# Optimization experiments

Hardware: AMD Instinct MI355X
Metric: run time of the kernel (lower is better)

Reference implementation:

```python
import jax, jax.numpy as jnp
import numpy as np

B, S, H, NH, L, NS = 8, 4096, 768, 12, 2, 64
DH = H // NH
EPS = 1e-12


def _layer_norm(x, g, b):
    mu = jnp.mean(x, axis=-1, keepdims=True)
    var = jnp.mean((x - mu) ** 2, axis=-1, keepdims=True)
    return (x - mu) / jnp.sqrt(var + EPS) * g + b


def setup_inputs() -> dict:
    key = jax.random.key(0)
    ks = jax.random.split(key, 8)
    # sentence index per token: 64 equal contiguous sentences; position 0 is [CLS] in sentence 0
    sent_ind = jnp.broadcast_to((jnp.arange(S, dtype=jnp.int32) * NS) // S, (B, S)).astype(jnp.int32)
    start_layer = jax.random.normal(ks[0], (B, S, H), dtype=jnp.float32)
    init = lambda k, shape: (jax.random.normal(k, shape, dtype=jnp.float32) * 0.02)
    return {
        "sent_ind": sent_ind,
        "start_layer": start_layer,
        "Wq": init(ks[1], (L, H, H)), "bq": jnp.zeros((L, H), jnp.float32),
        "Wk": init(ks[2], (L, H, H)), "bk": jnp.zeros((L, H), jnp.float32),
        "Wv": init(ks[3], (L, H, H)), "bv": jnp.zeros((L, H), jnp.float32),
        "Wo": init(ks[4], (L, H, H)), "bo": jnp.zeros((L, H), jnp.float32),
        "ln_g": jnp.ones((L, H), jnp.float32), "ln_b": jnp.zeros((L, H), jnp.float32),
    }


def reference(sent_ind, start_layer, Wq, bq, Wk, bk, Wv, bv, Wo, bo, ln_g, ln_b):
    # ---- segment-mean pooling by sentence index (vectorized replacement of the python loops) ----
    onehot = (sent_ind[..., None] == jnp.arange(NS, dtype=sent_ind.dtype)).astype(start_layer.dtype)  # [B,S,NS]
    # the first [CLS] token is excluded from sentence 0's mean
    onehot = onehot.at[:, 0, :].set(0.0)
    sums = jnp.einsum('bsn,bsd->bnd', onehot, start_layer)          # [B,NS,H]
    counts = jnp.sum(onehot, axis=1)                                 # [B,NS]
    x = sums / counts[..., None]                                     # graph_vectors [B,NS,H]

    # ---- GAT layers: BertSelfAttention + GATSelfOutput(dense->gelu->LayerNorm), dropout=eval ----
    scale = 1.0 / (DH ** 0.5)
    for i in range(L):
        q = (x @ Wq[i] + bq[i]).reshape(B, NS, NH, DH)
        k = (x @ Wk[i] + bk[i]).reshape(B, NS, NH, DH)
        v = (x @ Wv[i] + bv[i]).reshape(B, NS, NH, DH)
        scores = jnp.einsum('bqhd,bkhd->bhqk', q, k) * scale
        probs = jax.nn.softmax(scores, axis=-1)
        ctx = jnp.einsum('bhqk,bkhd->bqhd', probs, v).reshape(B, NS, H)
        h = jax.nn.gelu(ctx @ Wo[i] + bo[i], approximate=False)
        x = _layer_norm(h, ln_g[i], ln_b[i])
    return x
```

## Files before the change

kernel.cpp:

```cpp
#include <hip/hip_runtime.h>
#include <hip/hip_bf16.h>

constexpr int cB  = 8;
constexpr int cS  = 4096;
constexpr int cH  = 768;
constexpr int cNH = 12;
constexpr int cL  = 2;
constexpr int cNS = 64;
constexpr int cDH = 64;
constexpr int cM  = cB * cNS;

typedef __attribute__((ext_vector_type(8))) short bf16x8;
typedef __attribute__((ext_vector_type(4))) float f32x4;

union PrepShared {
    float T[64][65];
    struct { int cnt; int list[cS]; } p;
};

__global__ __launch_bounds__(256) void prep_kernel(
    const int* __restrict__ sent_ind, const float* __restrict__ sl,
    __hip_bfloat16* __restrict__ xb,
    const float* __restrict__ Wq, const float* __restrict__ Wk,
    const float* __restrict__ Wv, const float* __restrict__ Wo,
    __hip_bfloat16* __restrict__ wt)
{
    __shared__ PrepShared sh;
    int tid = threadIdx.x;

    if (blockIdx.x < (unsigned)cM) {
        int bn = blockIdx.x;
        int b = bn >> 6, n = bn & (cNS - 1);
        if (tid == 0) sh.p.cnt = 0;
        __syncthreads();
        const int* si = sent_ind + (size_t)b * cS;
        for (int s = tid; s < cS; s += 256)
            if (s != 0 && si[s] == n) { int p = atomicAdd(&sh.p.cnt, 1); sh.p.list[p] = s; }
        __syncthreads();
        int c = sh.p.cnt;
        if (tid < 192) {
            const float* bbase = sl + (size_t)b * cS * cH;
            int col = tid * 4;
            float4 a0 = {0.f, 0.f, 0.f, 0.f};
            float4 a1 = {0.f, 0.f, 0.f, 0.f};
            float4 a2 = {0.f, 0.f, 0.f, 0.f};
            float4 a3 = {0.f, 0.f, 0.f, 0.f};
            int i = 0;
            for (; i + 4 <= c; i += 4) {
                float4 r0 = *(const float4*)(bbase + (size_t)sh.p.list[i + 0] * cH + col);
                float4 r1 = *(const float4*)(bbase + (size_t)sh.p.list[i + 1] * cH + col);
                float4 r2 = *(const float4*)(bbase + (size_t)sh.p.list[i + 2] * cH + col);
                float4 r3 = *(const float4*)(bbase + (size_t)sh.p.list[i + 3] * cH + col);
                a0.x += r0.x; a0.y += r0.y; a0.z += r0.z; a0.w += r0.w;
                a1.x += r1.x; a1.y += r1.y; a1.z += r1.z; a1.w += r1.w;
                a2.x += r2.x; a2.y += r2.y; a2.z += r2.z; a2.w += r2.w;
                a3.x += r3.x; a3.y += r3.y; a3.z += r3.z; a3.w += r3.w;
            }
            for (; i < c; ++i) {
                float4 r0 = *(const float4*)(bbase + (size_t)sh.p.list[i] * cH + col);
                a0.x += r0.x; a0.y += r0.y; a0.z += r0.z; a0.w += r0.w;
            }
            float inv = 1.0f / (float)c;
            __hip_bfloat16* xr = xb + (size_t)bn * cH + col;
            xr[0] = __float2bfloat16((a0.x + a1.x + a2.x + a3.x) * inv);
            xr[1] = __float2bfloat16((a0.y + a1.y + a2.y + a3.y) * inv);
            xr[2] = __float2bfloat16((a0.z + a1.z + a2.z + a3.z) * inv);
            xr[3] = __float2bfloat16((a0.w + a1.w + a2.w + a3.w) * inv);
        }
    } else {
        int bi = blockIdx.x - cM;
        int bx = bi % 12, by = (bi / 12) % 12, mat = bi / 144;
        int layer = mat >> 2, which = mat & 3;
        const float* W = (which == 0 ? Wq : which == 1 ? Wk : which == 2 ? Wv : Wo)
                         + (size_t)layer * cH * cH;
        int k0 = by * 64, n0 = bx * 64;
        int r = tid >> 2, cb = (tid & 3) * 16;
        #pragma unroll
        for (int u = 0; u < 4; ++u) {
            float4 w4 = *(const float4*)(W + (size_t)(k0 + r) * cH + n0 + cb + u * 4);
            sh.T[r][cb + u * 4 + 0] = w4.x; sh.T[r][cb + u * 4 + 1] = w4.y;
            sh.T[r][cb + u * 4 + 2] = w4.z; sh.T[r][cb + u * 4 + 3] = w4.w;
        }
        __syncthreads();
        int kk = tid & 63;
        int nb = (tid >> 6) * 16;
        __hip_bfloat16* dst = wt + ((size_t)mat * cH + n0) * cH + k0;
        #pragma unroll
        for (int u = 0; u < 16; ++u) {
            int nn = nb + u;
            dst[(size_t)nn * cH + kk] = __float2bfloat16(sh.T[kk][nn]);
        }
    }
}

template<int ACT>
__global__ __launch_bounds__(256) void gemm_mfma(
    const __hip_bfloat16* __restrict__ A,
    const __hip_bfloat16* __restrict__ Wt0,
    const float* __restrict__ biasA, const float* __restrict__ biasB,
    const float* __restrict__ biasC,
    float* __restrict__ C0)
{
    constexpr int K = cH, N = cH;
    int mat = blockIdx.z;
    const __hip_bfloat16* Wt = Wt0 + (size_t)mat * cH * cH;
    const float* bias = (mat == 0) ? biasA : (mat == 1) ? biasB : biasC;
    float* C = C0 + (size_t)mat * cM * cH;

    int lane = threadIdx.x & 63;
    int wave = threadIdx.x >> 6;
    int l15 = lane & 15, q = lane >> 4;
    int m0 = blockIdx.y * 64 + wave * 16;
    int n0 = blockIdx.x * 32;

    const __hip_bfloat16* Arow = A  + (size_t)(m0 + l15) * K + q * 8;
    const __hip_bfloat16* Wr0  = Wt + (size_t)(n0 + l15) * K + q * 8;
    const __hip_bfloat16* Wr1  = Wr0 + (size_t)16 * K;

    f32x4 acc0 = {0.f, 0.f, 0.f, 0.f};
    f32x4 acc1 = {0.f, 0.f, 0.f, 0.f};
    #pragma unroll 8
    for (int k0 = 0; k0 < K; k0 += 32) {
        bf16x8 a  = *(const bf16x8*)(Arow + k0);
        bf16x8 b0 = *(const bf16x8*)(Wr0 + k0);
        bf16x8 b1 = *(const bf16x8*)(Wr1 + k0);
        acc0 = __builtin_amdgcn_mfma_f32_16x16x32_bf16(a, b0, acc0, 0, 0, 0);
        acc1 = __builtin_amdgcn_mfma_f32_16x16x32_bf16(a, b1, acc1, 0, 0, 0);
    }
    #pragma unroll
    for (int nt = 0; nt < 2; ++nt) {
        const f32x4 acc = nt == 0 ? acc0 : acc1;
        int col = n0 + nt * 16 + l15;
        float bv = bias[col];
        #pragma unroll
        for (int r = 0; r < 4; ++r) {
            int row = m0 + q * 4 + r;
            float v = acc[r] + bv;
            if (ACT == 1) v = 0.5f * v * (1.0f + erff(v * 0.70710678118654752f));
            C[(size_t)row * N + col] = v;
        }
    }
}

__global__ __launch_bounds__(256) void attn_kernel(
    const float* __restrict__ q, const float* __restrict__ k,
    const float* __restrict__ v, __hip_bfloat16* __restrict__ ctx)
{
    int bh = blockIdx.x;
    int b = bh / cNH, hh = bh % cNH;
    __shared__ float Qs[cNS][cDH + 4];
    __shared__ float Ks[cNS][cDH + 4];
    __shared__ float Vt[cDH][cNS + 4];
    __shared__ float Ps[cNS][cNS + 4];
    int tid = threadIdx.x;
    size_t base = ((size_t)b * cNS) * cH + hh * cDH;

    for (int i = tid; i < cNS * cDH / 4; i += 256) {
        int r = i >> 4;
        int c = (i & 15) << 2;
        float4 qv = *(const float4*)(q + base + (size_t)r * cH + c);
        float4 kv = *(const float4*)(k + base + (size_t)r * cH + c);
        float4 vv = *(const float4*)(v + base + (size_t)r * cH + c);
        *(float4*)&Qs[r][c] = qv;
        *(float4*)&Ks[r][c] = kv;
        Vt[c + 0][r] = vv.x; Vt[c + 1][r] = vv.y;
        Vt[c + 2][r] = vv.z; Vt[c + 3][r] = vv.w;
    }
    __syncthreads();

    int tx = tid & 15, ty = tid >> 4;
    float accs[4][4] = {};
    for (int d = 0; d < cDH; d += 4) {
        float4 qv[4], kv[4];
        #pragma unroll
        for (int i = 0; i < 4; ++i) qv[i] = *(const float4*)&Qs[ty * 4 + i][d];
        #pragma unroll
        for (int j = 0; j < 4; ++j) kv[j] = *(const float4*)&Ks[tx + j * 16][d];
        #pragma unroll
        for (int i = 0; i < 4; ++i)
            #pragma unroll
            for (int j = 0; j < 4; ++j)
                accs[i][j] += qv[i].x * kv[j].x + qv[i].y * kv[j].y +
                              qv[i].z * kv[j].z + qv[i].w * kv[j].w;
    }
    const float scale = 0.125f;
    #pragma unroll
    for (int i = 0; i < 4; ++i)
        #pragma unroll
        for (int j = 0; j < 4; ++j)
            Ps[ty * 4 + i][tx + j * 16] = accs[i][j] * scale;
    __syncthreads();

    {
        int row = tid >> 2, jq = tid & 3;
        float e[16];
        float m = -1e30f;
        #pragma unroll
        for (int c = 0; c < 16; ++c) { e[c] = Ps[row][jq * 16 + c]; m = fmaxf(m, e[c]); }
        m = fmaxf(m, __shfl_xor(m, 1));
        m = fmaxf(m, __shfl_xor(m, 2));
        float s = 0.f;
        #pragma unroll
        for (int c = 0; c < 16; ++c) { e[c] = __expf(e[c] - m); s += e[c]; }
        s += __shfl_xor(s, 1);
        s += __shfl_xor(s, 2);
        float inv = 1.0f / s;
        #pragma unroll
        for (int c = 0; c < 16; ++c) Ps[row][jq * 16 + c] = e[c] * inv;
    }
    __syncthreads();

    float acco[4][4] = {};
    for (int c = 0; c < cNS; c += 4) {
        float4 p4[4], vt4[4];
        #pragma unroll
        for (int i = 0; i < 4; ++i) p4[i] = *(const float4*)&Ps[ty * 4 + i][c];
        #pragma unroll
        for (int j = 0; j < 4; ++j) vt4[j] = *(const float4*)&Vt[tx + j * 16][c];
        #pragma unroll
        for (int i = 0; i < 4; ++i)
            #pragma unroll
            for (int j = 0; j < 4; ++j)
                acco[i][j] += p4[i].x * vt4[j].x + p4[i].y * vt4[j].y +
                              p4[i].z * vt4[j].z + p4[i].w * vt4[j].w;
    }
    #pragma unroll
    for (int i = 0; i < 4; ++i)
        #pragma unroll
        for (int j = 0; j < 4; ++j)
            ctx[base + (size_t)(ty * 4 + i) * cH + tx + j * 16] =
                __float2bfloat16(acco[i][j]);
}

__global__ __launch_bounds__(256) void ln_kernel(
    const float* __restrict__ h, const float* __restrict__ g,
    const float* __restrict__ bb, __hip_bfloat16* __restrict__ xb,
    float* __restrict__ outf)
{
    int row = blockIdx.x;
    const float* r = h + (size_t)row * cH;
    int tid = threadIdx.x;
    float v0 = r[tid], v1 = r[tid + 256], v2 = r[tid + 512];
    float s = v0 + v1 + v2;
    __shared__ float red[4];
    #pragma unroll
    for (int o = 32; o; o >>= 1) s += __shfl_xor(s, o);
    if ((tid & 63) == 0) red[tid >> 6] = s;
    __syncthreads();
    float mu = (red[0] + red[1] + red[2] + red[3]) * (1.0f / 768.0f);
    float d0 = v0 - mu, d1 = v1 - mu, d2 = v2 - mu;
    float ss = d0 * d0 + d1 * d1 + d2 * d2;
    __syncthreads();
    #pragma unroll
    for (int o = 32; o; o >>= 1) ss += __shfl_xor(ss, o);
    if ((tid & 63) == 0) red[tid >> 6] = ss;
    __syncthreads();
    float var = (red[0] + red[1] + red[2] + red[3]) * (1.0f / 768.0f);
    float inv = rsqrtf(var + 1e-12f);
    float o0 = d0 * inv * g[tid]       + bb[tid];
    float o1 = d1 * inv * g[tid + 256] + bb[tid + 256];
    float o2 = d2 * inv * g[tid + 512] + bb[tid + 512];
    __hip_bfloat16* xr = xb + (size_t)row * cH;
    xr[tid]       = __float2bfloat16(o0);
    xr[tid + 256] = __float2bfloat16(o1);
    xr[tid + 512] = __float2bfloat16(o2);
    if (outf) {
        float* orow = outf + (size_t)row * cH;
        orow[tid] = o0; orow[tid + 256] = o1; orow[tid + 512] = o2;
    }
}

extern "C" void kernel_launch(void* const* d_in, const int* in_sizes, int n_in,
                              void* d_out, int out_size, void* d_ws, size_t ws_size,
                              hipStream_t stream) {
    const int*   sent_ind = (const int*)d_in[0];
    const float* start    = (const float*)d_in[1];
    const float* Wq = (const float*)d_in[2];
    const float* bq = (const float*)d_in[3];
    const float* Wk = (const float*)d_in[4];
    const float* bk = (const float*)d_in[5];
    const float* Wv = (const float*)d_in[6];
    const float* bv = (const float*)d_in[7];
    const float* Wo = (const float*)d_in[8];
    const float* bo = (const float*)d_in[9];
    const float* ln_g = (const float*)d_in[10];
    const float* ln_b = (const float*)d_in[11];
    float* out = (float*)d_out;

    char* w = (char*)d_ws;
    __hip_bfloat16* wt     = (__hip_bfloat16*)w;
    __hip_bfloat16* x_bf   = (__hip_bfloat16*)(w + 9437184);
    __hip_bfloat16* ctx_bf = (__hip_bfloat16*)(w + 9437184 + 786432);
    float* qb = (float*)(w + 9437184 + 2 * 786432);
    float* hb = qb + (size_t)3 * cM * cH;

    prep_kernel<<<cM + 1152, 256, 0, stream>>>(sent_ind, start, x_bf,
                                               Wq, Wk, Wv, Wo, wt);

    for (int i = 0; i < cL; ++i) {
        const __hip_bfloat16* wtq = wt + (size_t)(i * 4 + 0) * cH * cH;
        const __hip_bfloat16* wto = wt + (size_t)(i * 4 + 3) * cH * cH;
        gemm_mfma<0><<<dim3(24, 8, 3), 256, 0, stream>>>(
            x_bf, wtq, bq + (size_t)i * cH, bk + (size_t)i * cH, bv + (size_t)i * cH, qb);
        attn_kernel<<<cB * cNH, 256, 0, stream>>>(
            qb, qb + (size_t)cM * cH, qb + (size_t)2 * cM * cH, ctx_bf);
        gemm_mfma<1><<<dim3(24, 8, 1), 256, 0, stream>>>(
            ctx_bf, wto, bo + (size_t)i * cH, nullptr, nullptr, hb);
        ln_kernel<<<cM, 256, 0, stream>>>(hb, ln_g + (size_t)i * cH, ln_b + (size_t)i * cH,
                                          x_bf, (i == cL - 1) ? out : nullptr);
    }
}
```

Baseline: 292.5 us.

## Fuse all stages into one persistent cooperative kernel with grid syncs

Replaces the prep, QKV GEMM, attention, output GEMM and LayerNorm launches with a single cooperative kernel of 256 blocks. Each phase loops over its work items and phases are separated by grid.sync, with one shared-memory union reused across phases. The aim is to remove per-launch overhead and the gaps between the nine kernels. The cost is that the bandwidth-heavy pooling and weight-transpose phase now runs on only 256 resident blocks instead of over 1600, which may hurt latency hiding. Grid-wide barriers also add their own cost.

```diff
diff --git a/kernel.cpp b/kernel.cpp
--- a/kernel.cpp
+++ b/kernel.cpp
@@ -1,5 +1,8 @@
 #include <hip/hip_runtime.h>
 #include <hip/hip_bf16.h>
+#include <hip/hip_cooperative_groups.h>
+
+namespace cg = cooperative_groups;
 
 constexpr int cB  = 8;
 constexpr int cS  = 4096;
@@ -9,118 +12,34 @@
 constexpr int cNS = 64;
 constexpr int cDH = 64;
 constexpr int cM  = cB * cNS;
+constexpr int cG  = 256;
 
 typedef __attribute__((ext_vector_type(8))) short bf16x8;
 typedef __attribute__((ext_vector_type(4))) float f32x4;
 
-union PrepShared {
+union SharedU {
+    struct { int cnt; int list[cS]; } p;
     float T[64][65];
-    struct { int cnt; int list[cS]; } p;
+    struct { float QP[64][68]; float Ks[64][68]; float Vt[64][68]; } a;
 };
 
-__global__ __launch_bounds__(256) void prep_kernel(
-    const int* __restrict__ sent_ind, const float* __restrict__ sl,
-    __hip_bfloat16* __restrict__ xb,
-    const float* __restrict__ Wq, const float* __restrict__ Wk,
-    const float* __restrict__ Wv, const float* __restrict__ Wo,
-    __hip_bfloat16* __restrict__ wt)
+__device__ inline void gemm_tile(const __hip_bfloat16* __restrict__ A,
+                                 const __hip_bfloat16* __restrict__ Wt,
+                                 const float* __restrict__ bias,
+                                 float* __restrict__ C,
+                                 int bx, int by, int l15, int q4, int wave,
+                                 bool gelu)
 {
-    __shared__ PrepShared sh;
-    int tid = threadIdx.x;
-
-    if (blockIdx.x < (unsigned)cM) {
-        int bn = blockIdx.x;
-        int b = bn >> 6, n = bn & (cNS - 1);
-        if (tid == 0) sh.p.cnt = 0;
-        __syncthreads();
-        const int* si = sent_ind + (size_t)b * cS;
-        for (int s = tid; s < cS; s += 256)
-            if (s != 0 && si[s] == n) { int p = atomicAdd(&sh.p.cnt, 1); sh.p.list[p] = s; }
-        __syncthreads();
-        int c = sh.p.cnt;
-        if (tid < 192) {
-            const float* bbase = sl + (size_t)b * cS * cH;
-            int col = tid * 4;
-            float4 a0 = {0.f, 0.f, 0.f, 0.f};
-            float4 a1 = {0.f, 0.f, 0.f, 0.f};
-            float4 a2 = {0.f, 0.f, 0.f, 0.f};
-            float4 a3 = {0.f, 0.f, 0.f, 0.f};
-            int i = 0;
-            for (; i + 4 <= c; i += 4) {
-                float4 r0 = *(const float4*)(bbase + (size_t)sh.p.list[i + 0] * cH + col);
-                float4 r1 = *(const float4*)(bbase + (size_t)sh.p.list[i + 1] * cH + col);
-                float4 r2 = *(const float4*)(bbase + (size_t)sh.p.list[i + 2] * cH + col);
-                float4 r3 = *(const float4*)(bbase + (size_t)sh.p.list[i + 3] * cH + col);
-                a0.x += r0.x; a0.y += r0.y; a0.z += r0.z; a0.w += r0.w;
-                a1.x += r1.x; a1.y += r1.y; a1.z += r1.z; a1.w += r1.w;
-                a2.x += r2.x; a2.y += r2.y; a2.z += r2.z; a2.w += r2.w;
-                a3.x += r3.x; a3.y += r3.y; a3.z += r3.z; a3.w += r3.w;
-            }
-            for (; i < c; ++i) {
-                float4 r0 = *(const float4*)(bbase + (size_t)sh.p.list[i] * cH + col);
-                a0.x += r0.x; a0.y += r0.y; a0.z += r0.z; a0.w += r0.w;
-            }
-            float inv = 1.0f / (float)c;
-            __hip_bfloat16* xr = xb + (size_t)bn * cH + col;
-            xr[0] = __float2bfloat16((a0.x + a1.x + a2.x + a3.x) * inv);
-            xr[1] = __float2bfloat16((a0.y + a1.y + a2.y + a3.y) * inv);
-            xr[2] = __float2bfloat16((a0.z + a1.z + a2.z + a3.z) * inv);
-            xr[3] = __float2bfloat16((a0.w + a1.w + a2.w + a3.w) * inv);
-        }
-    } else {
-        int bi = blockIdx.x - cM;
-        int bx = bi % 12, by = (bi / 12) % 12, mat = bi / 144;
-        int layer = mat >> 2, which = mat & 3;
-        const float* W = (which == 0 ? Wq : which == 1 ? Wk : which == 2 ? Wv : Wo)
-                         + (size_t)layer * cH * cH;
-        int k0 = by * 64, n0 = bx * 64;
-        int r = tid >> 2, cb = (tid & 3) * 16;
-        #pragma unroll
-        for (int u = 0; u < 4; ++u) {
-            float4 w4 = *(const float4*)(W + (size_t)(k0 + r) * cH + n0 + cb + u * 4);
-            sh.T[r][cb + u * 4 + 0] = w4.x; sh.T[r][cb + u * 4 + 1] = w4.y;
-            sh.T[r][cb + u * 4 + 2] = w4.z; sh.T[r][cb + u * 4 + 3] = w4.w;
-        }
-        __syncthreads();
-        int kk = tid & 63;
-        int nb = (tid >> 6) * 16;
-        __hip_bfloat16* dst = wt + ((size_t)mat * cH + n0) * cH + k0;
-        #pragma unroll
-        for (int u = 0; u < 16; ++u) {
-            int nn = nb + u;
-            dst[(size_t)nn * cH + kk] = __float2bfloat16(sh.T[kk][nn]);
-        }
-    }
-}
-
-template<int ACT>
-__global__ __launch_bounds__(256) void gemm_mfma(
-    const __hip_bfloat16* __restrict__ A,
-    const __hip_bfloat16* __restrict__ Wt0,
-    const float* __restrict__ biasA, const float* __restrict__ biasB,
-    const float* __restrict__ biasC,
-    float* __restrict__ C0)
-{
-    constexpr int K = cH, N = cH;
-    int mat = blockIdx.z;
-    const __hip_bfloat16* Wt = Wt0 + (size_t)mat * cH * cH;
-    const float* bias = (mat == 0) ? biasA : (mat == 1) ? biasB : biasC;
-    float* C = C0 + (size_t)mat * cM * cH;
-
-    int lane = threadIdx.x & 63;
-    int wave = threadIdx.x >> 6;
-    int l15 = lane & 15, q = lane >> 4;
-    int m0 = blockIdx.y * 64 + wave * 16;
-    int n0 = blockIdx.x * 32;
-
-    const __hip_bfloat16* Arow = A  + (size_t)(m0 + l15) * K + q * 8;
-    const __hip_bfloat16* Wr0  = Wt + (size_t)(n0 + l15) * K + q * 8;
-    const __hip_bfloat16* Wr1  = Wr0 + (size_t)16 * K;
+    int m0 = by * 64 + wave * 16;
+    int n0 = bx * 32;
+    const __hip_bfloat16* Arow = A  + (size_t)(m0 + l15) * cH + q4 * 8;
+    const __hip_bfloat16* Wr0  = Wt + (size_t)(n0 + l15) * cH + q4 * 8;
+    const __hip_bfloat16* Wr1  = Wr0 + (size_t)16 * cH;
 
     f32x4 acc0 = {0.f, 0.f, 0.f, 0.f};
     f32x4 acc1 = {0.f, 0.f, 0.f, 0.f};
     #pragma unroll 8
-    for (int k0 = 0; k0 < K; k0 += 32) {
+    for (int k0 = 0; k0 < cH; k0 += 32) {
         bf16x8 a  = *(const bf16x8*)(Arow + k0);
         bf16x8 b0 = *(const bf16x8*)(Wr0 + k0);
         bf16x8 b1 = *(const bf16x8*)(Wr1 + k0);
@@ -134,25 +53,21 @@
         float bv = bias[col];
         #pragma unroll
         for (int r = 0; r < 4; ++r) {
-            int row = m0 + q * 4 + r;
             float v = acc[r] + bv;
-            if (ACT == 1) v = 0.5f * v * (1.0f + erff(v * 0.70710678118654752f));
-            C[(size_t)row * N + col] = v;
+            if (gelu) v = 0.5f * v * (1.0f + erff(v * 0.70710678118654752f));
+            C[(size_t)(m0 + q4 * 4 + r) * cH + col] = v;
         }
     }
 }
 
-__global__ __launch_bounds__(256) void attn_kernel(
-    const float* __restrict__ q, const float* __restrict__ k,
-    const float* __restrict__ v, __hip_bfloat16* __restrict__ ctx)
+__device__ inline void attn_item(SharedU& sh, const float* __restrict__ qb,
+                                 __hip_bfloat16* __restrict__ ctx_bf,
+                                 int bh, int tid)
 {
-    int bh = blockIdx.x;
+    const float* q = qb;
+    const float* k = qb + (size_t)cM * cH;
+    const float* v = qb + (size_t)2 * cM * cH;
     int b = bh / cNH, hh = bh % cNH;
-    __shared__ float Qs[cNS][cDH + 4];
-    __shared__ float Ks[cNS][cDH + 4];
-    __shared__ float Vt[cDH][cNS + 4];
-    __shared__ float Ps[cNS][cNS + 4];
-    int tid = threadIdx.x;
     size_t base = ((size_t)b * cNS) * cH + hh * cDH;
 
     for (int i = tid; i < cNS * cDH / 4; i += 256) {
@@ -161,10 +76,10 @@
         float4 qv = *(const float4*)(q + base + (size_t)r * cH + c);
         float4 kv = *(const float4*)(k + base + (size_t)r * cH + c);
         float4 vv = *(const float4*)(v + base + (size_t)r * cH + c);
-        *(float4*)&Qs[r][c] = qv;
-        *(float4*)&Ks[r][c] = kv;
-        Vt[c + 0][r] = vv.x; Vt[c + 1][r] = vv.y;
-        Vt[c + 2][r] = vv.z; Vt[c + 3][r] = vv.w;
+        *(float4*)&sh.a.QP[r][c] = qv;
+        *(float4*)&sh.a.Ks[r][c] = kv;
+        sh.a.Vt[c + 0][r] = vv.x; sh.a.Vt[c + 1][r] = vv.y;
+        sh.a.Vt[c + 2][r] = vv.z; sh.a.Vt[c + 3][r] = vv.w;
     }
     __syncthreads();
 
@@ -173,9 +88,9 @@
     for (int d = 0; d < cDH; d += 4) {
         float4 qv[4], kv[4];
         #pragma unroll
-        for (int i = 0; i < 4; ++i) qv[i] = *(const float4*)&Qs[ty * 4 + i][d];
-        #pragma unroll
-        for (int j = 0; j < 4; ++j) kv[j] = *(const float4*)&Ks[tx + j * 16][d];
+        for (int i = 0; i < 4; ++i) qv[i] = *(const float4*)&sh.a.QP[ty * 4 + i][d];
+        #pragma unroll
+        for (int j = 0; j < 4; ++j) kv[j] = *(const float4*)&sh.a.Ks[tx + j * 16][d];
         #pragma unroll
         for (int i = 0; i < 4; ++i)
             #pragma unroll
@@ -183,12 +98,13 @@
                 accs[i][j] += qv[i].x * kv[j].x + qv[i].y * kv[j].y +
                               qv[i].z * kv[j].z + qv[i].w * kv[j].w;
     }
+    __syncthreads();
     const float scale = 0.125f;
     #pragma unroll
     for (int i = 0; i < 4; ++i)
         #pragma unroll
         for (int j = 0; j < 4; ++j)
-            Ps[ty * 4 + i][tx + j * 16] = accs[i][j] * scale;
+            sh.a.QP[ty * 4 + i][tx + j * 16] = accs[i][j] * scale;
     __syncthreads();
 
     {
@@ -196,7 +112,7 @@
         float e[16];
         float m = -1e30f;
         #pragma unroll
-        for (int c = 0; c < 16; ++c) { e[c] = Ps[row][jq * 16 + c]; m = fmaxf(m, e[c]); }
+        for (int c = 0; c < 16; ++c) { e[c] = sh.a.QP[row][jq * 16 + c]; m = fmaxf(m, e[c]); }
         m = fmaxf(m, __shfl_xor(m, 1));
         m = fmaxf(m, __shfl_xor(m, 2));
         float s = 0.f;
@@ -206,7 +122,7 @@
         s += __shfl_xor(s, 2);
         float inv = 1.0f / s;
         #pragma unroll
-        for (int c = 0; c < 16; ++c) Ps[row][jq * 16 + c] = e[c] * inv;
+        for (int c = 0; c < 16; ++c) sh.a.QP[row][jq * 16 + c] = e[c] * inv;
     }
     __syncthreads();
 
@@ -214,9 +130,9 @@
     for (int c = 0; c < cNS; c += 4) {
         float4 p4[4], vt4[4];
         #pragma unroll
-        for (int i = 0; i < 4; ++i) p4[i] = *(const float4*)&Ps[ty * 4 + i][c];
-        #pragma unroll
-        for (int j = 0; j < 4; ++j) vt4[j] = *(const float4*)&Vt[tx + j * 16][c];
+        for (int i = 0; i < 4; ++i) p4[i] = *(const float4*)&sh.a.QP[ty * 4 + i][c];
+        #pragma unroll
+        for (int j = 0; j < 4; ++j) vt4[j] = *(const float4*)&sh.a.Vt[tx + j * 16][c];
         #pragma unroll
         for (int i = 0; i < 4; ++i)
             #pragma unroll
@@ -228,45 +144,154 @@
     for (int i = 0; i < 4; ++i)
         #pragma unroll
         for (int j = 0; j < 4; ++j)
-            ctx[base + (size_t)(ty * 4 + i) * cH + tx + j * 16] =
+            ctx_bf[base + (size_t)(ty * 4 + i) * cH + tx + j * 16] =
                 __float2bfloat16(acco[i][j]);
 }
 
-__global__ __launch_bounds__(256) void ln_kernel(
-    const float* __restrict__ h, const float* __restrict__ g,
-    const float* __restrict__ bb, __hip_bfloat16* __restrict__ xb,
-    float* __restrict__ outf)
+__global__ __launch_bounds__(256) void fused_kernel(
+    const int* __restrict__ sent_ind, const float* __restrict__ sl,
+    const float* __restrict__ Wq, const float* __restrict__ Wk,
+    const float* __restrict__ Wv, const float* __restrict__ Wo,
+    const float* __restrict__ bq, const float* __restrict__ bk,
+    const float* __restrict__ bv, const float* __restrict__ bo,
+    const float* __restrict__ ln_g, const float* __restrict__ ln_b,
+    __hip_bfloat16* __restrict__ wt, __hip_bfloat16* __restrict__ x_bf,
+    __hip_bfloat16* __restrict__ ctx_bf,
+    float* __restrict__ qb, float* __restrict__ hb, float* __restrict__ out)
 {
-    int row = blockIdx.x;
-    const float* r = h + (size_t)row * cH;
+    __shared__ SharedU sh;
+    __shared__ float red[4];
+    cg::grid_group grid = cg::this_grid();
     int tid = threadIdx.x;
-    float v0 = r[tid], v1 = r[tid + 256], v2 = r[tid + 512];
-    float s = v0 + v1 + v2;
-    __shared__ float red[4];
-    #pragma unroll
-    for (int o = 32; o; o >>= 1) s += __shfl_xor(s, o);
-    if ((tid & 63) == 0) red[tid >> 6] = s;
-    __syncthreads();
-    float mu = (red[0] + red[1] + red[2] + red[3]) * (1.0f / 768.0f);
-    float d0 = v0 - mu, d1 = v1 - mu, d2 = v2 - mu;
-    float ss = d0 * d0 + d1 * d1 + d2 * d2;
-    __syncthreads();
-    #pragma unroll
-    for (int o = 32; o; o >>= 1) ss += __shfl_xor(ss, o);
-    if ((tid & 63) == 0) red[tid >> 6] = ss;
-    __syncthreads();
-    float var = (red[0] + red[1] + red[2] + red[3]) * (1.0f / 768.0f);
-    float inv = rsqrtf(var + 1e-12f);
-    float o0 = d0 * inv * g[tid]       + bb[tid];
-    float o1 = d1 * inv * g[tid + 256] + bb[tid + 256];
-    float o2 = d2 * inv * g[tid + 512] + bb[tid + 512];
-    __hip_bfloat16* xr = xb + (size_t)row * cH;
-    xr[tid]       = __float2bfloat16(o0);
-    xr[tid + 256] = __float2bfloat16(o1);
-    xr[tid + 512] = __float2bfloat16(o2);
-    if (outf) {
-        float* orow = outf + (size_t)row * cH;
-        orow[tid] = o0; orow[tid + 256] = o1; orow[tid + 512] = o2;
+    int lane = tid & 63, wave = tid >> 6;
+    int l15 = lane & 15, q4 = lane >> 4;
+
+    for (int it = blockIdx.x; it < cM + 1152; it += cG) {
+        __syncthreads();
+        if (it < cM) {
+            int bn = it, b = bn >> 6, n = bn & (cNS - 1);
+            if (tid == 0) sh.p.cnt = 0;
+            __syncthreads();
+            const int* si = sent_ind + (size_t)b * cS;
+            for (int s = tid; s < cS; s += 256)
+                if (s != 0 && si[s] == n) { int p = atomicAdd(&sh.p.cnt, 1); sh.p.list[p] = s; }
+            __syncthreads();
+            int c = sh.p.cnt;
+            if (tid < 192) {
+                const float* bbase = sl + (size_t)b * cS * cH;
+                int col = tid * 4;
+                float4 a0 = {0.f, 0.f, 0.f, 0.f};
+                float4 a1 = {0.f, 0.f, 0.f, 0.f};
+                float4 a2 = {0.f, 0.f, 0.f, 0.f};
+                float4 a3 = {0.f, 0.f, 0.f, 0.f};
+                int i = 0;
+                for (; i + 4 <= c; i += 4) {
+                    float4 r0 = *(const float4*)(bbase + (size_t)sh.p.list[i + 0] * cH + col);
+                    float4 r1 = *(const float4*)(bbase + (size_t)sh.p.list[i + 1] * cH + col);
+                    float4 r2 = *(const float4*)(bbase + (size_t)sh.p.list[i + 2] * cH + col);
+                    float4 r3 = *(const float4*)(bbase + (size_t)sh.p.list[i + 3] * cH + col);
+                    a0.x += r0.x; a0.y += r0.y; a0.z += r0.z; a0.w += r0.w;
+                    a1.x += r1.x; a1.y += r1.y; a1.z += r1.z; a1.w += r1.w;
+                    a2.x += r2.x; a2.y += r2.y; a2.z += r2.z; a2.w += r2.w;
+                    a3.x += r3.x; a3.y += r3.y; a3.z += r3.z; a3.w += r3.w;
+                }
+                for (; i < c; ++i) {
+                    float4 r0 = *(const float4*)(bbase + (size_t)sh.p.list[i] * cH + col);
+                    a0.x += r0.x; a0.y += r0.y; a0.z += r0.z; a0.w += r0.w;
+                }
+                float inv = 1.0f / (float)c;
+                __hip_bfloat16* xr = x_bf + (size_t)bn * cH + col;
+                xr[0] = __float2bfloat16((a0.x + a1.x + a2.x + a3.x) * inv);
+                xr[1] = __float2bfloat16((a0.y + a1.y + a2.y + a3.y) * inv);
+                xr[2] = __float2bfloat16((a0.z + a1.z + a2.z + a3.z) * inv);
+                xr[3] = __float2bfloat16((a0.w + a1.w + a2.w + a3.w) * inv);
+            }
+        } else {
+            int bi = it - cM;
+            int bx = bi % 12, by = (bi / 12) % 12, mat = bi / 144;
+            int layer = mat >> 2, which = mat & 3;
+            const float* W = (which == 0 ? Wq : which == 1 ? Wk : which == 2 ? Wv : Wo)
+                             + (size_t)layer * cH * cH;
+            int k0 = by * 64, n0 = bx * 64;
+            int r = tid >> 2, cb = (tid & 3) * 16;
+            #pragma unroll
+            for (int u = 0; u < 4; ++u) {
+                float4 w4 = *(const float4*)(W + (size_t)(k0 + r) * cH + n0 + cb + u * 4);
+                sh.T[r][cb + u * 4 + 0] = w4.x; sh.T[r][cb + u * 4 + 1] = w4.y;
+                sh.T[r][cb + u * 4 + 2] = w4.z; sh.T[r][cb + u * 4 + 3] = w4.w;
+            }
+            __syncthreads();
+            int kk = tid & 63;
+            int nb = (tid >> 6) * 16;
+            __hip_bfloat16* dst = wt + ((size_t)mat * cH + n0) * cH + k0;
+            #pragma unroll
+            for (int u = 0; u < 16; ++u) {
+                int nn = nb + u;
+                dst[(size_t)nn * cH + kk] = __float2bfloat16(sh.T[kk][nn]);
+            }
+        }
+    }
+    grid.sync();
+
+    for (int layer = 0; layer < cL; ++layer) {
+        const __hip_bfloat16* wqkv = wt + (size_t)(layer * 4) * cH * cH;
+        const __hip_bfloat16* wto  = wt + (size_t)(layer * 4 + 3) * cH * cH;
+
+        for (int it = blockIdx.x; it < 576; it += cG) {
+            int bx = it % 24, by = (it / 24) % 8, mat = it / 192;
+            const __hip_bfloat16* Wt = wqkv + (size_t)mat * cH * cH;
+            const float* bias = (mat == 0 ? bq : mat == 1 ? bk : bv) + (size_t)layer * cH;
+            gemm_tile(x_bf, Wt, bias, qb + (size_t)mat * cM * cH,
+                      bx, by, l15, q4, wave, false);
+        }
+        grid.sync();
+
+        for (int it = blockIdx.x; it < cB * cNH; it += cG)
+            attn_item(sh, qb, ctx_bf, it, tid);
+        grid.sync();
+
+        for (int it = blockIdx.x; it < 192; it += cG) {
+            int bx = it % 24, by = it / 24;
+            gemm_tile(ctx_bf, wto, bo + (size_t)layer * cH, hb,
+                      bx, by, l15, q4, wave, true);
+        }
+        grid.sync();
+
+        const float* g  = ln_g + (size_t)layer * cH;
+        const float* bb = ln_b + (size_t)layer * cH;
+        float* outf = (layer == cL - 1) ? out : nullptr;
+        for (int row = blockIdx.x; row < cM; row += cG) {
+            __syncthreads();
+            const float* r = hb + (size_t)row * cH;
+            float v0 = r[tid], v1 = r[tid + 256], v2 = r[tid + 512];
+            float s = v0 + v1 + v2;
+            #pragma unroll
+            for (int o = 32; o; o >>= 1) s += __shfl_xor(s, o);
+            if ((tid & 63) == 0) red[tid >> 6] = s;
+            __syncthreads();
+            float mu = (red[0] + red[1] + red[2] + red[3]) * (1.0f / 768.0f);
+            float d0 = v0 - mu, d1 = v1 - mu, d2 = v2 - mu;
+            float ss = d0 * d0 + d1 * d1 + d2 * d2;
+            __syncthreads();
+            #pragma unroll
+            for (int o = 32; o; o >>= 1) ss += __shfl_xor(ss, o);
+            if ((tid & 63) == 0) red[tid >> 6] = ss;
+            __syncthreads();
+            float var = (red[0] + red[1] + red[2] + red[3]) * (1.0f / 768.0f);
+            float inv = rsqrtf(var + 1e-12f);
+            float o0 = d0 * inv * g[tid]       + bb[tid];
+            float o1 = d1 * inv * g[tid + 256] + bb[tid + 256];
+            float o2 = d2 * inv * g[tid + 512] + bb[tid + 512];
+            __hip_bfloat16* xr = x_bf + (size_t)row * cH;
+            xr[tid]       = __float2bfloat16(o0);
+            xr[tid + 256] = __float2bfloat16(o1);
+            xr[tid + 512] = __float2bfloat16(o2);
+            if (outf) {
+                float* orow = outf + (size_t)row * cH;
+                orow[tid] = o0; orow[tid + 256] = o1; orow[tid + 512] = o2;
+            }
+        }
+        grid.sync();
     }
 }
 
@@ -294,19 +319,14 @@
     float* qb = (float*)(w + 9437184 + 2 * 786432);
     float* hb = qb + (size_t)3 * cM * cH;
 
-    prep_kernel<<<cM + 1152, 256, 0, stream>>>(sent_ind, start, x_bf,
-                                               Wq, Wk, Wv, Wo, wt);
-
-    for (int i = 0; i < cL; ++i) {
-        const __hip_bfloat16* wtq = wt + (size_t)(i * 4 + 0) * cH * cH;
-        const __hip_bfloat16* wto = wt + (size_t)(i * 4 + 3) * cH * cH;
-        gemm_mfma<0><<<dim3(24, 8, 3), 256, 0, stream>>>(
-            x_bf, wtq, bq + (size_t)i * cH, bk + (size_t)i * cH, bv + (size_t)i * cH, qb);
-        attn_kernel<<<cB * cNH, 256, 0, stream>>>(
-            qb, qb + (size_t)cM * cH, qb + (size_t)2 * cM * cH, ctx_bf);
-        gemm_mfma<1><<<dim3(24, 8, 1), 256, 0, stream>>>(
-            ctx_bf, wto, bo + (size_t)i * cH, nullptr, nullptr, hb);
-        ln_kernel<<<cM, 256, 0, stream>>>(hb, ln_g + (size_t)i * cH, ln_b + (size_t)i * cH,
-                                          x_bf, (i == cL - 1) ? out : nullptr);
-    }
+    void* args[] = {
+        (void*)&sent_ind, (void*)&start,
+        (void*)&Wq, (void*)&Wk, (void*)&Wv, (void*)&Wo,
+        (void*)&bq, (void*)&bk, (void*)&bv, (void*)&bo,
+        (void*)&ln_g, (void*)&ln_b,
+        (void*)&wt, (void*)&x_bf, (void*)&ctx_bf,
+        (void*)&qb, (void*)&hb, (void*)&out,
+    };
+    hipLaunchCooperativeKernel((void*)fused_kernel, dim3(cG), dim3(256),
+                               args, 0, stream);
 }
```

New measurement: 596.4 us. +103.9%, slower.

## Fuse QKV projection into attention and output projection with GELU and LayerNorm

Applied to the files above, without the earlier changes.

Replaces the separate QKV GEMM plus attention kernels with one kernel per (batch, head) that computes that head's Q/K/V slice with MFMA directly into shared memory, then runs attention. Also fuses the output projection, GELU and LayerNorm into one kernel computing 16 full rows per block, using a single-pass sum/sum-of-squares variance. This removes the fp32 intermediate Q/K/V/h buffers and two launches per layer. In exchange, grid sizes drop to 96 and 32 blocks, which may underfill the GPU, and the variance formula changes numerically.

```diff
diff --git a/kernel.cpp b/kernel.cpp
--- a/kernel.cpp
+++ b/kernel.cpp
@@ -93,78 +93,77 @@
     }
 }
 
-template<int ACT>
-__global__ __launch_bounds__(256) void gemm_mfma(
-    const __hip_bfloat16* __restrict__ A,
-    const __hip_bfloat16* __restrict__ Wt0,
-    const float* __restrict__ biasA, const float* __restrict__ biasB,
-    const float* __restrict__ biasC,
-    float* __restrict__ C0)
+struct AttnShared {
+    float QP[cNS][cDH + 4];
+    float Ks[cNS][cDH + 4];
+    float Vt[cDH][cNS + 4];
+};
+
+__global__ __launch_bounds__(256) void qkvattn_kernel(
+    const __hip_bfloat16* __restrict__ x_bf,
+    const __hip_bfloat16* __restrict__ wqkv,
+    const float* __restrict__ bq, const float* __restrict__ bk,
+    const float* __restrict__ bv,
+    __hip_bfloat16* __restrict__ ctx_bf)
 {
-    constexpr int K = cH, N = cH;
-    int mat = blockIdx.z;
-    const __hip_bfloat16* Wt = Wt0 + (size_t)mat * cH * cH;
-    const float* bias = (mat == 0) ? biasA : (mat == 1) ? biasB : biasC;
-    float* C = C0 + (size_t)mat * cM * cH;
-
-    int lane = threadIdx.x & 63;
-    int wave = threadIdx.x >> 6;
-    int l15 = lane & 15, q = lane >> 4;
-    int m0 = blockIdx.y * 64 + wave * 16;
-    int n0 = blockIdx.x * 32;
-
-    const __hip_bfloat16* Arow = A  + (size_t)(m0 + l15) * K + q * 8;
-    const __hip_bfloat16* Wr0  = Wt + (size_t)(n0 + l15) * K + q * 8;
-    const __hip_bfloat16* Wr1  = Wr0 + (size_t)16 * K;
-
-    f32x4 acc0 = {0.f, 0.f, 0.f, 0.f};
-    f32x4 acc1 = {0.f, 0.f, 0.f, 0.f};
-    #pragma unroll 8
-    for (int k0 = 0; k0 < K; k0 += 32) {
-        bf16x8 a  = *(const bf16x8*)(Arow + k0);
-        bf16x8 b0 = *(const bf16x8*)(Wr0 + k0);
-        bf16x8 b1 = *(const bf16x8*)(Wr1 + k0);
-        acc0 = __builtin_amdgcn_mfma_f32_16x16x32_bf16(a, b0, acc0, 0, 0, 0);
-        acc1 = __builtin_amdgcn_mfma_f32_16x16x32_bf16(a, b1, acc1, 0, 0, 0);
-    }
-    #pragma unroll
-    for (int nt = 0; nt < 2; ++nt) {
-        const f32x4 acc = nt == 0 ? acc0 : acc1;
-        int col = n0 + nt * 16 + l15;
-        float bv = bias[col];
-        #pragma unroll
-        for (int r = 0; r < 4; ++r) {
-            int row = m0 + q * 4 + r;
-            float v = acc[r] + bv;
-            if (ACT == 1) v = 0.5f * v * (1.0f + erff(v * 0.70710678118654752f));
-            C[(size_t)row * N + col] = v;
-        }
-    }
-}
-
-__global__ __launch_bounds__(256) void attn_kernel(
-    const float* __restrict__ q, const float* __restrict__ k,
-    const float* __restrict__ v, __hip_bfloat16* __restrict__ ctx)
-{
-    int bh = blockIdx.x;
-    int b = bh / cNH, hh = bh % cNH;
-    __shared__ float Qs[cNS][cDH + 4];
-    __shared__ float Ks[cNS][cDH + 4];
-    __shared__ float Vt[cDH][cNS + 4];
-    __shared__ float Ps[cNS][cNS + 4];
+    __shared__ AttnShared sh;
     int tid = threadIdx.x;
-    size_t base = ((size_t)b * cNS) * cH + hh * cDH;
-
-    for (int i = tid; i < cNS * cDH / 4; i += 256) {
-        int r = i >> 4;
-        int c = (i & 15) << 2;
-        float4 qv = *(const float4*)(q + base + (size_t)r * cH + c);
-        float4 kv = *(const float4*)(k + base + (size_t)r * cH + c);
-        float4 vv = *(const float4*)(v + base + (size_t)r * cH + c);
-        *(float4*)&Qs[r][c] = qv;
-        *(float4*)&Ks[r][c] = kv;
-        Vt[c + 0][r] = vv.x; Vt[c + 1][r] = vv.y;
-        Vt[c + 2][r] = vv.z; Vt[c + 3][r] = vv.w;
+    int lane = tid & 63, wave = tid >> 6;
+    int l15 = lane & 15, q4 = lane >> 4;
+    int b = blockIdx.x / cNH, hh = blockIdx.x % cNH;
+
+    const __hip_bfloat16* Arow[4];
+    #pragma unroll
+    for (int m = 0; m < 4; ++m)
+        Arow[m] = x_bf + (size_t)(b * 64 + m * 16 + l15) * cH + q4 * 8;
+    const __hip_bfloat16* Brow[3];
+    int cmat[3], cnt_[3];
+    #pragma unroll
+    for (int j = 0; j < 3; ++j) {
+        int c = wave * 3 + j;
+        cmat[j] = c >> 2; cnt_[j] = c & 3;
+        Brow[j] = wqkv + (size_t)cmat[j] * cH * cH
+                       + (size_t)(hh * 64 + cnt_[j] * 16 + l15) * cH + q4 * 8;
+    }
+
+    f32x4 acc[3][4];
+    #pragma unroll
+    for (int j = 0; j < 3; ++j)
+        #pragma unroll
+        for (int m = 0; m < 4; ++m) acc[j][m] = (f32x4){0.f, 0.f, 0.f, 0.f};
+
+    #pragma unroll 4
+    for (int k0 = 0; k0 < cH; k0 += 32) {
+        bf16x8 a[4], bb8[3];
+        #pragma unroll
+        for (int m = 0; m < 4; ++m) a[m] = *(const bf16x8*)(Arow[m] + k0);
+        #pragma unroll
+        for (int j = 0; j < 3; ++j) bb8[j] = *(const bf16x8*)(Brow[j] + k0);
+        #pragma unroll
+        for (int j = 0; j < 3; ++j)
+            #pragma unroll
+            for (int m = 0; m < 4; ++m)
+                acc[j][m] = __builtin_amdgcn_mfma_f32_16x16x32_bf16(a[m], bb8[j], acc[j][m], 0, 0, 0);
+    }
+
+    const float scale = 0.125f;
+    #pragma unroll
+    for (int j = 0; j < 3; ++j) {
+        int mat = cmat[j], nt = cnt_[j];
+        int col_d = nt * 16 + l15;
+        int col_g = hh * 64 + col_d;
+        float bias = (mat == 0 ? bq : mat == 1 ? bk : bv)[col_g];
+        #pragma unroll
+        for (int m = 0; m < 4; ++m) {
+            #pragma unroll
+            for (int r = 0; r < 4; ++r) {
+                int row_s = m * 16 + q4 * 4 + r;
+                float v = acc[j][m][r] + bias;
+                if (mat == 0)      sh.QP[row_s][col_d] = v * scale;
+                else if (mat == 1) sh.Ks[row_s][col_d] = v;
+                else               sh.Vt[col_d][row_s] = v;
+            }
+        }
     }
     __syncthreads();
 
@@ -173,9 +172,9 @@
     for (int d = 0; d < cDH; d += 4) {
         float4 qv[4], kv[4];
         #pragma unroll
-        for (int i = 0; i < 4; ++i) qv[i] = *(const float4*)&Qs[ty * 4 + i][d];
-        #pragma unroll
-        for (int j = 0; j < 4; ++j) kv[j] = *(const float4*)&Ks[tx + j * 16][d];
+        for (int i = 0; i < 4; ++i) qv[i] = *(const float4*)&sh.QP[ty * 4 + i][d];
+        #pragma unroll
+        for (int j = 0; j < 4; ++j) kv[j] = *(const float4*)&sh.Ks[tx + j * 16][d];
         #pragma unroll
         for (int i = 0; i < 4; ++i)
             #pragma unroll
@@ -183,12 +182,12 @@
                 accs[i][j] += qv[i].x * kv[j].x + qv[i].y * kv[j].y +
                               qv[i].z * kv[j].z + qv[i].w * kv[j].w;
     }
-    const float scale = 0.125f;
+    __syncthreads();
     #pragma unroll
     for (int i = 0; i < 4; ++i)
         #pragma unroll
         for (int j = 0; j < 4; ++j)
-            Ps[ty * 4 + i][tx + j * 16] = accs[i][j] * scale;
+            sh.QP[ty * 4 + i][tx + j * 16] = accs[i][j];
     __syncthreads();
 
     {
@@ -196,7 +195,7 @@
         float e[16];
         float m = -1e30f;
         #pragma unroll
-        for (int c = 0; c < 16; ++c) { e[c] = Ps[row][jq * 16 + c]; m = fmaxf(m, e[c]); }
+        for (int c = 0; c < 16; ++c) { e[c] = sh.QP[row][jq * 16 + c]; m = fmaxf(m, e[c]); }
         m = fmaxf(m, __shfl_xor(m, 1));
         m = fmaxf(m, __shfl_xor(m, 2));
         float s = 0.f;
@@ -206,7 +205,7 @@
         s += __shfl_xor(s, 2);
         float inv = 1.0f / s;
         #pragma unroll
-        for (int c = 0; c < 16; ++c) Ps[row][jq * 16 + c] = e[c] * inv;
+        for (int c = 0; c < 16; ++c) sh.QP[row][jq * 16 + c] = e[c] * inv;
     }
     __syncthreads();
 
@@ -214,9 +213,9 @@
     for (int c = 0; c < cNS; c += 4) {
         float4 p4[4], vt4[4];
         #pragma unroll
-        for (int i = 0; i < 4; ++i) p4[i] = *(const float4*)&Ps[ty * 4 + i][c];
-        #pragma unroll
-        for (int j = 0; j < 4; ++j) vt4[j] = *(const float4*)&Vt[tx + j * 16][c];
+        for (int i = 0; i < 4; ++i) p4[i] = *(const float4*)&sh.QP[ty * 4 + i][c];
+        #pragma unroll
+        for (int j = 0; j < 4; ++j) vt4[j] = *(const float4*)&sh.Vt[tx + j * 16][c];
         #pragma unroll
         for (int i = 0; i < 4; ++i)
             #pragma unroll
@@ -224,49 +223,94 @@
                 acco[i][j] += p4[i].x * vt4[j].x + p4[i].y * vt4[j].y +
                               p4[i].z * vt4[j].z + p4[i].w * vt4[j].w;
     }
+    size_t base = ((size_t)b * cNS) * cH + hh * cDH;
     #pragma unroll
     for (int i = 0; i < 4; ++i)
         #pragma unroll
         for (int j = 0; j < 4; ++j)
-            ctx[base + (size_t)(ty * 4 + i) * cH + tx + j * 16] =
+            ctx_bf[base + (size_t)(ty * 4 + i) * cH + tx + j * 16] =
                 __float2bfloat16(acco[i][j]);
 }
 
-__global__ __launch_bounds__(256) void ln_kernel(
-    const float* __restrict__ h, const float* __restrict__ g,
-    const float* __restrict__ bb, __hip_bfloat16* __restrict__ xb,
-    float* __restrict__ outf)
+__global__ __launch_bounds__(256) void oln_kernel(
+    const __hip_bfloat16* __restrict__ ctx_bf,
+    const __hip_bfloat16* __restrict__ wto,
+    const float* __restrict__ bo,
+    const float* __restrict__ g, const float* __restrict__ bb,
+    __hip_bfloat16* __restrict__ xb, float* __restrict__ outf)
 {
-    int row = blockIdx.x;
-    const float* r = h + (size_t)row * cH;
+    __shared__ float part[4][16][2];
     int tid = threadIdx.x;
-    float v0 = r[tid], v1 = r[tid + 256], v2 = r[tid + 512];
-    float s = v0 + v1 + v2;
-    __shared__ float red[4];
-    #pragma unroll
-    for (int o = 32; o; o >>= 1) s += __shfl_xor(s, o);
-    if ((tid & 63) == 0) red[tid >> 6] = s;
-    __syncthreads();
-    float mu = (red[0] + red[1] + red[2] + red[3]) * (1.0f / 768.0f);
-    float d0 = v0 - mu, d1 = v1 - mu, d2 = v2 - mu;
-    float ss = d0 * d0 + d1 * d1 + d2 * d2;
-    __syncthreads();
-    #pragma unroll
-    for (int o = 32; o; o >>= 1) ss += __shfl_xor(ss, o);
-    if ((tid & 63) == 0) red[tid >> 6] = ss;
-    __syncthreads();
-    float var = (red[0] + red[1] + red[2] + red[3]) * (1.0f / 768.0f);
-    float inv = rsqrtf(var + 1e-12f);
-    float o0 = d0 * inv * g[tid]       + bb[tid];
-    float o1 = d1 * inv * g[tid + 256] + bb[tid + 256];
-    float o2 = d2 * inv * g[tid + 512] + bb[tid + 512];
-    __hip_bfloat16* xr = xb + (size_t)row * cH;
-    xr[tid]       = __float2bfloat16(o0);
-    xr[tid + 256] = __float2bfloat16(o1);
-    xr[tid + 512] = __float2bfloat16(o2);
-    if (outf) {
-        float* orow = outf + (size_t)row * cH;
-        orow[tid] = o0; orow[tid + 256] = o1; orow[tid + 512] = o2;
+    int lane = tid & 63, wave = tid >> 6;
+    int l15 = lane & 15, q4 = lane >> 4;
+    int r0 = blockIdx.x * 16;
+
+    const __hip_bfloat16* Arow = ctx_bf + (size_t)(r0 + l15) * cH + q4 * 8;
+    const __hip_bfloat16* Brow[12];
+    #pragma unroll
+    for (int nt = 0; nt < 12; ++nt)
+        Brow[nt] = wto + (size_t)(wave * 192 + nt * 16 + l15) * cH + q4 * 8;
+
+    f32x4 acc[12];
+    #pragma unroll
+    for (int nt = 0; nt < 12; ++nt) acc[nt] = (f32x4){0.f, 0.f, 0.f, 0.f};
+
+    #pragma unroll 2
+    for (int k0 = 0; k0 < cH; k0 += 32) {
+        bf16x8 a = *(const bf16x8*)(Arow + k0);
+        #pragma unroll
+        for (int nt = 0; nt < 12; ++nt) {
+            bf16x8 b8 = *(const bf16x8*)(Brow[nt] + k0);
+            acc[nt] = __builtin_amdgcn_mfma_f32_16x16x32_bf16(a, b8, acc[nt], 0, 0, 0);
+        }
+    }
+
+    float rs[4] = {0.f, 0.f, 0.f, 0.f}, rq[4] = {0.f, 0.f, 0.f, 0.f};
+    #pragma unroll
+    for (int nt = 0; nt < 12; ++nt) {
+        int col = wave * 192 + nt * 16 + l15;
+        float bv = bo[col];
+        #pragma unroll
+        for (int r = 0; r < 4; ++r) {
+            float v = acc[nt][r] + bv;
+            v = 0.5f * v * (1.0f + erff(v * 0.70710678118654752f));
+            acc[nt][r] = v;
+            rs[r] += v;
+            rq[r] += v * v;
+        }
+    }
+    #pragma unroll
+    for (int o = 8; o; o >>= 1) {
+        #pragma unroll
+        for (int r = 0; r < 4; ++r) {
+            rs[r] += __shfl_xor(rs[r], o);
+            rq[r] += __shfl_xor(rq[r], o);
+        }
+    }
+    if (l15 == 0) {
+        #pragma unroll
+        for (int r = 0; r < 4; ++r) {
+            part[wave][q4 * 4 + r][0] = rs[r];
+            part[wave][q4 * 4 + r][1] = rq[r];
+        }
+    }
+    __syncthreads();
+    #pragma unroll
+    for (int r = 0; r < 4; ++r) {
+        int row = q4 * 4 + r;
+        float S  = part[0][row][0] + part[1][row][0] + part[2][row][0] + part[3][row][0];
+        float Q2 = part[0][row][1] + part[1][row][1] + part[2][row][1] + part[3][row][1];
+        float mu  = S * (1.0f / 768.0f);
+        float var = Q2 * (1.0f / 768.0f) - mu * mu;
+        float inv = rsqrtf(var + 1e-12f);
+        int row_g = r0 + row;
+        #pragma unroll
+        for (int nt = 0; nt < 12; ++nt) {
+            int col = wave * 192 + nt * 16 + l15;
+            float o = (acc[nt][r] - mu) * inv * g[col] + bb[col];
+            xb[(size_t)row_g * cH + col] = __float2bfloat16(o);
+            if (outf) outf[(size_t)row_g * cH + col] = o;
+        }
     }
 }
 
@@ -291,22 +335,19 @@
     __hip_bfloat16* wt     = (__hip_bfloat16*)w;
     __hip_bfloat16* x_bf   = (__hip_bfloat16*)(w + 9437184);
     __hip_bfloat16* ctx_bf = (__hip_bfloat16*)(w + 9437184 + 786432);
-    float* qb = (float*)(w + 9437184 + 2 * 786432);
-    float* hb = qb + (size_t)3 * cM * cH;
 
     prep_kernel<<<cM + 1152, 256, 0, stream>>>(sent_ind, start, x_bf,
                                                Wq, Wk, Wv, Wo, wt);
 
     for (int i = 0; i < cL; ++i) {
-        const __hip_bfloat16* wtq = wt + (size_t)(i * 4 + 0) * cH * cH;
-        const __hip_bfloat16* wto = wt + (size_t)(i * 4 + 3) * cH * cH;
-        gemm_mfma<0><<<dim3(24, 8, 3), 256, 0, stream>>>(
-            x_bf, wtq, bq + (size_t)i * cH, bk + (size_t)i * cH, bv + (size_t)i * cH, qb);
-        attn_kernel<<<cB * cNH, 256, 0, stream>>>(
-            qb, qb + (size_t)cM * cH, qb + (size_t)2 * cM * cH, ctx_bf);
-        gemm_mfma<1><<<dim3(24, 8, 1), 256, 0, stream>>>(
-            ctx_bf, wto, bo + (size_t)i * cH, nullptr, nullptr, hb);
-        ln_kernel<<<cM, 256, 0, stream>>>(hb, ln_g + (size_t)i * cH, ln_b + (size_t)i * cH,
-                                          x_bf, (i == cL - 1) ? out : nullptr);
+        const __hip_bfloat16* wqkv = wt + (size_t)(i * 4) * cH * cH;
+        const __hip_bfloat16* wto  = wt + (size_t)(i * 4 + 3) * cH * cH;
+        qkvattn_kernel<<<cB * cNH, 256, 0, stream>>>(
+            x_bf, wqkv, bq + (size_t)i * cH, bk + (size_t)i * cH, bv + (size_t)i * cH,
+            ctx_bf);
+        oln_kernel<<<cM / 16, 256, 0, stream>>>(
+            ctx_bf, wto, bo + (size_t)i * cH,
+            ln_g + (size_t)i * cH, ln_b + (size_t)i * cH,
+            x_bf, (i == cL - 1) ? out : nullptr);
     }
 }
```

After: 350.3 us. +19.8%, slower.
